# Kernel tuning notes

Measured on AMD Instinct MI355X. Metric: run time of the kernel, lower is better.

The kernel has to match this reference:

```python
import jax, jax.numpy as jnp
import numpy as np


def setup_inputs() -> dict:
    key = jax.random.key(0)
    k1, k2, k3 = jax.random.split(key, 3)
    B, S, IN, OUT = 4, 2048, 4096, 4096
    # int8 activations, weights, bias (stored as int8; math accumulates in int32)
    x = jax.random.randint(k1, (B, S, IN), -127, 128, dtype=jnp.int32).astype(jnp.int8)
    weight = jax.random.randint(k2, (OUT, IN), -127, 128, dtype=jnp.int32).astype(jnp.int8)  # (out, in)
    bias = jax.random.randint(k3, (1, OUT), -127, 128, dtype=jnp.int32).astype(jnp.int8)
    alpha = jnp.float32(0.001)  # input_scale*weight_scale/output_scale
    beta = jnp.float32(0.01)    # bias_scale/output_scale
    return {"x": x, "weight": weight, "bias": bias, "alpha": alpha, "beta": beta}


def reference(x, weight, bias, alpha, beta):
    # Flatten leading dims: (B,S,IN) -> (N,IN)
    x_shape = x.shape
    xf = x.reshape(-1, x_shape[-1])
    acc = jax.lax.dot_general(
        xf, weight,
        dimension_numbers=(((1,), (1,)), ((), ())),
        preferred_element_type=jnp.int32,
    )  # (N, OUT) int32
    # Fused epilogue: y = round(alpha*acc + beta*bias), saturate to int8
    yf = alpha * acc.astype(jnp.float32) + beta * bias.astype(jnp.float32)
    y = jnp.clip(jnp.round(yf), -128.0, 127.0).astype(jnp.int8)
    return y.reshape(*x_shape[:-1], -1)
```

## Files before the change

### kernel.cpp

```cpp
#include <hip/hip_runtime.h>
#include <stdint.h>

using i32x4  = __attribute__((ext_vector_type(4)))  int;
using i32x16 = __attribute__((ext_vector_type(16))) int;

#define M_TOT 8192
#define N_TOT 4096
#define K_TOT 4096
#define BM 256
#define BN 256
#define NTILES 32

__device__ __forceinline__ void gload_lds16(const void* g, void* l) {
  __builtin_amdgcn_global_load_lds(
      (const __attribute__((address_space(1))) void*)(uintptr_t)g,
      (__attribute__((address_space(3))) void*)(uint32_t)(uintptr_t)l,
      16, 0, 0);
}

__global__ void pack_tiles(const int* __restrict__ a32, const int* __restrict__ b32,
                           int8_t* __restrict__ ap, int8_t* __restrict__ bp,
                           int na, int ntot) {
  int stride = gridDim.x * blockDim.x;
  for (int idx = blockIdx.x * blockDim.x + threadIdx.x; idx < ntot; idx += stride) {
    int i = idx;
    const int* src;
    int8_t* dst;
    if (idx < na) { src = a32; dst = ap; }
    else          { src = b32; dst = bp; i = idx - na; }
    int sp = i & 7;
    int rr = (i >> 3) & 255;
    int kt = (i >> 11) & 31;
    int p  = i >> 16;
    int sl = sp ^ (rr & 7);
    const i32x4* s = (const i32x4*)(src + ((size_t)(p * 256 + rr)) * 4096 + (kt * 8 + sl) * 16);
    i32x4 a = s[0], b = s[1], c = s[2], d = s[3];
    i32x4 o;
    o.x = (a.x & 255) | ((a.y & 255) << 8) | ((a.z & 255) << 16) | (a.w << 24);
    o.y = (b.x & 255) | ((b.y & 255) << 8) | ((b.z & 255) << 16) | (b.w << 24);
    o.z = (c.x & 255) | ((c.y & 255) << 8) | ((c.z & 255) << 16) | (c.w << 24);
    o.w = (d.x & 255) | ((d.y & 255) << 8) | ((d.z & 255) << 16) | (d.w << 24);
    ((i32x4*)dst)[idx < na ? i : i] = o;
    ((i32x4*)dst)[i] = o;
  }
}

#define STAGE_T(kt, BUF) {                                                  \
    const int8_t* _ga = Asrc + ((size_t)(kt) << 15) + stoff;                \
    char* _da = lds + ((BUF) << 15) + stoff;                                \
    gload_lds16(_ga, _da);               gload_lds16(_ga + 1024, _da + 1024); \
    gload_lds16(_ga + 2048, _da + 2048); gload_lds16(_ga + 3072, _da + 3072); \
    const int8_t* _gb = Bsrc + ((size_t)(kt) << 15) + stoff;                \
    char* _db = lds + 65536 + ((BUF) << 15) + stoff;                        \
    gload_lds16(_gb, _db);               gload_lds16(_gb + 1024, _db + 1024); \
    gload_lds16(_gb + 2048, _db + 2048); gload_lds16(_gb + 3072, _db + 3072); }

#define LOAD_FRAGS(DA, DB, BUF, S) {                                        \
    const int _so = ((((S) << 1) | hi) ^ sx) * 16;                          \
    const char* _pa = lds + ((BUF) << 15) + _so;                            \
    const char* _pb = _pa + 65536;                                          \
    _Pragma("unroll")                                                       \
    for (int mi = 0; mi < 4; ++mi) DA[mi] = *(const i32x4*)(_pa + aRow[mi]); \
    _Pragma("unroll")                                                       \
    for (int ni = 0; ni < 2; ++ni) DB[ni] = *(const i32x4*)(_pb + bRow[ni]); }

#define MFMA8(A, B)                                                         \
    _Pragma("unroll")                                                       \
    for (int mi = 0; mi < 4; ++mi)                                          \
    _Pragma("unroll")                                                       \
    for (int ni = 0; ni < 2; ++ni)                                          \
      acc[mi][ni] = __builtin_amdgcn_mfma_i32_32x32x32_i8(A[mi], B[ni], acc[mi][ni], 0, 0, 0);

#define SGB(m, n) __builtin_amdgcn_sched_group_barrier((m), (n), 0)
#define PAIR SGB(0x8, 1); SGB(0x100, 1);
#define KSBLOCK PAIR PAIR PAIR PAIR PAIR PAIR SGB(0x8, 2);

#define INTERVAL(kt, BUF, DO_STAGE) {                                       \
    asm volatile("s_waitcnt vmcnt(0)" ::: "memory");                        \
    __builtin_amdgcn_s_barrier();                                           \
    __builtin_amdgcn_sched_barrier(0);                                      \
    __builtin_amdgcn_s_setprio(1);                                          \
    if (DO_STAGE) STAGE_T((kt) + 1, (BUF) ^ 1);                             \
    LOAD_FRAGS(a0, b0, BUF, 0)                                              \
    LOAD_FRAGS(a1, b1, BUF, 1)                                              \
    MFMA8(a0, b0)                                                           \
    LOAD_FRAGS(a0, b0, BUF, 2)                                              \
    MFMA8(a1, b1)                                                           \
    LOAD_FRAGS(a1, b1, BUF, 3)                                              \
    MFMA8(a0, b0)                                                           \
    MFMA8(a1, b1)                                                           \
    SGB(0x10, 8);                                                           \
    SGB(0x100, 6);                                                          \
    KSBLOCK KSBLOCK KSBLOCK                                                 \
    SGB(0x8, 8);                                                            \
    __builtin_amdgcn_s_setprio(0); }

__global__ __launch_bounds__(512, 2) void gemm_w8a8(
    const int8_t* __restrict__ Apack,
    const int8_t* __restrict__ Bpack,
    const int*    __restrict__ bias,
    const float*  __restrict__ alphap,
    const float*  __restrict__ betap,
    int* __restrict__ out)
{
  __shared__ __align__(16) char lds[131072];

  const int bid = blockIdx.x;
  const int xcd = bid & 7, wi = bid >> 3;
  const int tm = (xcd & 3) * 8 + (wi & 7);
  const int tn = (xcd >> 2) * 8 + (wi >> 3);

  const int tid = threadIdx.x;
  const int w   = tid >> 6;
  const int l   = tid & 63;
  const int lr  = l & 31;
  const int hi  = l >> 5;
  const int wr  = w >> 2;
  const int wc  = w & 3;
  const int stoff = w * 4096 + l * 16;
  const int sx  = lr & 7;

  const int8_t* Asrc = Apack + ((size_t)tm << 20);
  const int8_t* Bsrc = Bpack + ((size_t)tn << 20);

  int aRow[4], bRow[2];
#pragma unroll
  for (int mi = 0; mi < 4; ++mi) aRow[mi] = (wr * 128 + mi * 32 + lr) * 128;
#pragma unroll
  for (int ni = 0; ni < 2; ++ni) bRow[ni] = (wc * 64 + ni * 32 + lr) * 128;

  i32x16 acc[4][2] = {};
  i32x4 a0[4], b0[2], a1[4], b1[2];

  STAGE_T(0, 0)

  for (int tt = 0; tt < 15; ++tt) {
    const int k0 = tt * 2;
    INTERVAL(k0 + 0, 0, 1)
    INTERVAL(k0 + 1, 1, 1)
  }
  INTERVAL(30, 0, 1)
  INTERVAL(31, 1, 0)

  const float alpha = *alphap;
  const float beta  = *betap;
  const int brow = tm * BM, bcol = tn * BN;
#pragma unroll
  for (int ni = 0; ni < 2; ++ni) {
    const int col = bcol + wc * 64 + ni * 32 + lr;
    const float bb = beta * (float)bias[col];
#pragma unroll
    for (int mi = 0; mi < 4; ++mi) {
      const int rbase = brow + wr * 128 + mi * 32 + 4 * hi;
#pragma unroll
      for (int r = 0; r < 16; ++r) {
        const int row = rbase + (r & 3) + 8 * (r >> 2);
        float v = alpha * (float)acc[mi][ni][r] + bb;
        v = rintf(v);
        v = fminf(127.f, fmaxf(-128.f, v));
        out[(size_t)row * N_TOT + col] = (int)v;
      }
    }
  }
}

extern "C" void kernel_launch(void* const* d_in, const int* in_sizes, int n_in,
                              void* d_out, int out_size, void* d_ws, size_t ws_size,
                              hipStream_t stream) {
  const int*   x32    = (const int*)d_in[0];
  const int*   w32    = (const int*)d_in[1];
  const int*   bias   = (const int*)d_in[2];
  const float* alphap = (const float*)d_in[3];
  const float* betap  = (const float*)d_in[4];
  int* out = (int*)d_out;

  int8_t* xp = (int8_t*)d_ws;
  int8_t* wp = xp + (size_t)M_TOT * K_TOT;

  const int na   = (M_TOT * K_TOT) / 16;
  const int ntot = na + (N_TOT * K_TOT) / 16;
  pack_tiles<<<3072, 256, 0, stream>>>(x32, w32, xp, wp, na, ntot);

  gemm_w8a8<<<512, 512, 0, stream>>>(xp, wp, bias, alphap, betap, out);
}
```

Measured before the change: 190.5 us.

## Switch to 256x128 tiles with 4 waves and triple-buffered 64-wide K stages

Shrinks the output tile to 256x128 and the block to 256 threads, doubling the grid to 1024 blocks. The K step drops to 64 and the LDS ring now holds three stages, so waits use vmcnt(6) instead of draining to zero and global loads overlap compute. The pack kernel is rewritten to a 64-byte chunk layout with a new swizzle, and a redundant store is removed. In exchange each block rereads more of A relative to its output, and there are twice as many barrier intervals per tile.

```diff
diff --git a/kernel.cpp b/kernel.cpp
--- a/kernel.cpp
+++ b/kernel.cpp
@@ -8,8 +8,7 @@
 #define N_TOT 4096
 #define K_TOT 4096
 #define BM 256
-#define BN 256
-#define NTILES 32
+#define BN 128
 
 __device__ __forceinline__ void gload_lds16(const void* g, void* l) {
   __builtin_amdgcn_global_load_lds(
@@ -28,37 +27,35 @@
     int8_t* dst;
     if (idx < na) { src = a32; dst = ap; }
     else          { src = b32; dst = bp; i = idx - na; }
-    int sp = i & 7;
-    int rr = (i >> 3) & 255;
-    int kt = (i >> 11) & 31;
+    int sp = i & 3;
+    int rr = (i >> 2) & 255;
+    int kc = (i >> 10) & 63;
     int p  = i >> 16;
-    int sl = sp ^ (rr & 7);
-    const i32x4* s = (const i32x4*)(src + ((size_t)(p * 256 + rr)) * 4096 + (kt * 8 + sl) * 16);
+    int sl = sp ^ ((rr >> 1) & 3);
+    const i32x4* s = (const i32x4*)(src + (((size_t)(p * 256 + rr)) << 12) + kc * 64 + sl * 16);
     i32x4 a = s[0], b = s[1], c = s[2], d = s[3];
     i32x4 o;
     o.x = (a.x & 255) | ((a.y & 255) << 8) | ((a.z & 255) << 16) | (a.w << 24);
     o.y = (b.x & 255) | ((b.y & 255) << 8) | ((b.z & 255) << 16) | (b.w << 24);
     o.z = (c.x & 255) | ((c.y & 255) << 8) | ((c.z & 255) << 16) | (c.w << 24);
     o.w = (d.x & 255) | ((d.y & 255) << 8) | ((d.z & 255) << 16) | (d.w << 24);
-    ((i32x4*)dst)[idx < na ? i : i] = o;
     ((i32x4*)dst)[i] = o;
   }
 }
 
-#define STAGE_T(kt, BUF) {                                                  \
-    const int8_t* _ga = Asrc + ((size_t)(kt) << 15) + stoff;                \
-    char* _da = lds + ((BUF) << 15) + stoff;                                \
+#define STAGE(kc, R) {                                                     \
+    const int8_t* _ga = Asrc + (size_t)(kc) * 16384 + w * 4096 + l * 16;   \
+    char* _da = lds + (R) * 16384 + w * 4096 + l * 16;                     \
     gload_lds16(_ga, _da);               gload_lds16(_ga + 1024, _da + 1024); \
     gload_lds16(_ga + 2048, _da + 2048); gload_lds16(_ga + 3072, _da + 3072); \
-    const int8_t* _gb = Bsrc + ((size_t)(kt) << 15) + stoff;                \
-    char* _db = lds + 65536 + ((BUF) << 15) + stoff;                        \
-    gload_lds16(_gb, _db);               gload_lds16(_gb + 1024, _db + 1024); \
-    gload_lds16(_gb + 2048, _db + 2048); gload_lds16(_gb + 3072, _db + 3072); }
+    const int8_t* _gb = Bsrc + (size_t)(kc) * 16384 + w * 2048 + l * 16;   \
+    char* _db = lds + 49152 + (R) * 8192 + w * 2048 + l * 16;              \
+    gload_lds16(_gb, _db);               gload_lds16(_gb + 1024, _db + 1024); }
 
-#define LOAD_FRAGS(DA, DB, BUF, S) {                                        \
-    const int _so = ((((S) << 1) | hi) ^ sx) * 16;                          \
-    const char* _pa = lds + ((BUF) << 15) + _so;                            \
-    const char* _pb = _pa + 65536;                                          \
+#define LOAD_FRAGS(DA, DB, R, S) {                                          \
+    const int _so = ((((S) << 1) | hi) ^ swz) * 16;                         \
+    const char* _pa = lds + (R) * 16384 + _so;                              \
+    const char* _pb = lds + 49152 + (R) * 8192 + _so;                       \
     _Pragma("unroll")                                                       \
     for (int mi = 0; mi < 4; ++mi) DA[mi] = *(const i32x4*)(_pa + aRow[mi]); \
     _Pragma("unroll")                                                       \
@@ -73,29 +70,24 @@
 
 #define SGB(m, n) __builtin_amdgcn_sched_group_barrier((m), (n), 0)
 #define PAIR SGB(0x8, 1); SGB(0x100, 1);
-#define KSBLOCK PAIR PAIR PAIR PAIR PAIR PAIR SGB(0x8, 2);
 
-#define INTERVAL(kt, BUF, DO_STAGE) {                                       \
-    asm volatile("s_waitcnt vmcnt(0)" ::: "memory");                        \
+#define INTERVAL(kc2, R, RS, VM, DO_STAGE) {                                \
+    asm volatile("s_waitcnt vmcnt(" VM ")" ::: "memory");                   \
     __builtin_amdgcn_s_barrier();                                           \
     __builtin_amdgcn_sched_barrier(0);                                      \
     __builtin_amdgcn_s_setprio(1);                                          \
-    if (DO_STAGE) STAGE_T((kt) + 1, (BUF) ^ 1);                             \
-    LOAD_FRAGS(a0, b0, BUF, 0)                                              \
-    LOAD_FRAGS(a1, b1, BUF, 1)                                              \
+    if (DO_STAGE) STAGE(kc2, RS)                                            \
+    LOAD_FRAGS(a0, b0, R, sf)                                               \
     MFMA8(a0, b0)                                                           \
-    LOAD_FRAGS(a0, b0, BUF, 2)                                              \
+    LOAD_FRAGS(a1, b1, R, ss)                                               \
     MFMA8(a1, b1)                                                           \
-    LOAD_FRAGS(a1, b1, BUF, 3)                                              \
-    MFMA8(a0, b0)                                                           \
-    MFMA8(a1, b1)                                                           \
-    SGB(0x10, 8);                                                           \
     SGB(0x100, 6);                                                          \
-    KSBLOCK KSBLOCK KSBLOCK                                                 \
-    SGB(0x8, 8);                                                            \
+    SGB(0x10, 6);                                                           \
+    PAIR PAIR PAIR PAIR PAIR PAIR                                           \
+    SGB(0x8, 10);                                                           \
     __builtin_amdgcn_s_setprio(0); }
 
-__global__ __launch_bounds__(512, 2) void gemm_w8a8(
+__global__ __launch_bounds__(256, 2) void gemm_w8a8(
     const int8_t* __restrict__ Apack,
     const int8_t* __restrict__ Bpack,
     const int*    __restrict__ bias,
@@ -103,44 +95,49 @@
     const float*  __restrict__ betap,
     int* __restrict__ out)
 {
-  __shared__ __align__(16) char lds[131072];
+  __shared__ __align__(16) char lds[73728];
 
   const int bid = blockIdx.x;
   const int xcd = bid & 7, wi = bid >> 3;
   const int tm = (xcd & 3) * 8 + (wi & 7);
-  const int tn = (xcd >> 2) * 8 + (wi >> 3);
+  const int tn = (xcd >> 2) * 16 + (wi >> 3);
 
   const int tid = threadIdx.x;
   const int w   = tid >> 6;
   const int l   = tid & 63;
   const int lr  = l & 31;
   const int hi  = l >> 5;
-  const int wr  = w >> 2;
-  const int wc  = w & 3;
-  const int stoff = w * 4096 + l * 16;
-  const int sx  = lr & 7;
+  const int wr  = w >> 1;
+  const int wc  = w & 1;
+  const int sf  = w & 1;
+  const int ss  = sf ^ 1;
 
   const int8_t* Asrc = Apack + ((size_t)tm << 20);
-  const int8_t* Bsrc = Bpack + ((size_t)tn << 20);
+  const int8_t* Bsrc = Bpack + ((size_t)(tn >> 1) << 20) + (tn & 1) * 8192;
 
+  const int swz = (lr >> 1) & 3;
   int aRow[4], bRow[2];
 #pragma unroll
-  for (int mi = 0; mi < 4; ++mi) aRow[mi] = (wr * 128 + mi * 32 + lr) * 128;
+  for (int mi = 0; mi < 4; ++mi) aRow[mi] = (wr * 128 + mi * 32 + lr) * 64;
 #pragma unroll
-  for (int ni = 0; ni < 2; ++ni) bRow[ni] = (wc * 64 + ni * 32 + lr) * 128;
+  for (int ni = 0; ni < 2; ++ni) bRow[ni] = (wc * 64 + ni * 32 + lr) * 64;
 
   i32x16 acc[4][2] = {};
   i32x4 a0[4], b0[2], a1[4], b1[2];
 
-  STAGE_T(0, 0)
+  STAGE(0, 0)
+  STAGE(1, 1)
 
-  for (int tt = 0; tt < 15; ++tt) {
-    const int k0 = tt * 2;
-    INTERVAL(k0 + 0, 0, 1)
-    INTERVAL(k0 + 1, 1, 1)
+  for (int t = 0; t < 20; ++t) {
+    const int j = t * 3;
+    INTERVAL(j + 2, 0, 2, "6", 1)
+    INTERVAL(j + 3, 1, 0, "6", 1)
+    INTERVAL(j + 4, 2, 1, "6", 1)
   }
-  INTERVAL(30, 0, 1)
-  INTERVAL(31, 1, 0)
+  INTERVAL(62, 0, 2, "6", 1)
+  INTERVAL(63, 1, 0, "6", 1)
+  INTERVAL(0,  2, 0, "6", 0)
+  INTERVAL(0,  0, 0, "0", 0)
 
   const float alpha = *alphap;
   const float beta  = *betap;
@@ -181,5 +178,6 @@
   const int ntot = na + (N_TOT * K_TOT) / 16;
   pack_tiles<<<3072, 256, 0, stream>>>(x32, w32, xp, wp, na, ntot);
 
-  gemm_w8a8<<<512, 512, 0, stream>>>(xp, wp, bias, alphap, betap, out);
+  gemm_w8a8<<<dim3((M_TOT / BM) * (N_TOT / BN)), dim3(256), 0, stream>>>(
+      xp, wp, bias, alphap, betap, out);
 }
```

Result: slower. 207.4 us (+8.9%).
